# Kernel optimization log

Hardware: AMD Instinct MI355X
Metric: run time of the kernel (lower is better)

## Reference

```python
import jax, jax.numpy as jnp
import numpy as np

N, L, C, K = 8, 16384, 256, 64  # batch, points, d_color, anchor_num; d_struct = 4*K = 256


def setup_inputs() -> dict:
    key = jax.random.key(0)
    ks = jax.random.split(key, 12)
    d_in = C + 4 * K  # 512
    s1, s2, s3 = 1.0 / np.sqrt(d_in), 1.0 / np.sqrt(128), 1.0 / np.sqrt(256)
    return {
        'feat0': jax.random.normal(ks[0], (N, L, C), jnp.float32),
        'feat1': jax.random.normal(ks[1], (N, L, C), jnp.float32),
        'pts_3d0': jax.random.normal(ks[2], (N, L, 3), jnp.float32),
        'pts_3d1': jax.random.normal(ks[3], (N, L, 3), jnp.float32),
        'anchor_i': jax.random.randint(ks[4], (N, K), 0, L, jnp.int32),
        'anchor_j': jax.random.randint(ks[5], (N, K), 0, L, jnp.int32),
        'W1': jax.random.uniform(ks[6], (d_in, 128), jnp.float32, -s1, s1),
        'b1': jax.random.uniform(ks[7], (128,), jnp.float32, -s1, s1),
        'W2': jax.random.uniform(ks[8], (128, 256), jnp.float32, -s2, s2),
        'b2': jax.random.uniform(ks[9], (256,), jnp.float32, -s2, s2),
        'W3': jax.random.uniform(ks[10], (256, C), jnp.float32, -s3, s3),
        'b3': jax.random.uniform(ks[11], (C,), jnp.float32, -s3, s3),
    }


def _structured(pts, anchor_idx):
    # pts: [N,L,3], anchor_idx: [N,K] -> [N,L,4K]
    anchors = jnp.take_along_axis(pts, anchor_idx[:, :, None], axis=1)  # [N,K,3]
    diff = pts[:, :, None, :] - anchors[:, None, :, :]                  # [N,L,K,3]
    dist = jnp.sum(diff * diff, axis=-1, keepdims=True)                 # [N,L,K,1]
    f = jnp.concatenate([diff, dist], axis=-1)                          # [N,L,K,4]
    f = f / jnp.sum(jnp.abs(f), axis=-2, keepdims=True)                 # L1 norm over K
    f = jnp.swapaxes(f, -1, -2).reshape(pts.shape[0], pts.shape[1], -1)  # [N,L,4K]
    # original l1_norm is @torch.no_grad -> structured feature is detached
    return jax.lax.stop_gradient(f)


def _mlp(x, W1, b1, W2, b2, W3, b3):
    h = jax.nn.relu(x @ W1 + b1)
    h = jax.nn.relu(h @ W2 + b2)  # dropout is identity in eval
    return h @ W3 + b3


def reference(feat0, feat1, pts_3d0, pts_3d1, anchor_i, anchor_j,
              W1, b1, W2, b2, W3, b3):
    s0 = _structured(pts_3d0, anchor_i)
    s1 = _structured(pts_3d1, anchor_j)
    aug0 = _mlp(jnp.concatenate([feat0, s0], axis=-1), W1, b1, W2, b2, W3, b3)
    aug1 = _mlp(jnp.concatenate([feat1, s1], axis=-1), W1, b1, W2, b2, W3, b3)
    return aug0, aug1
```

## Files before the change

kernel.cpp:

```cpp
#include <hip/hip_runtime.h>

typedef __bf16 bf16x8 __attribute__((ext_vector_type(8)));
typedef float f32x4 __attribute__((ext_vector_type(4)));
typedef unsigned short u16x4 __attribute__((ext_vector_type(4)));

#define NBATCH 8
#define LPTS   16384
#define CDIM   256
#define KANC   64
#define DIN    512
#define H1DIM  128
#define H2DIM  256
#define TM     64
#define XSTR   320

__device__ __forceinline__ unsigned short f2b(float f){
  __bf16 h = (__bf16)f;
  return __builtin_bit_cast(unsigned short, h);
}

#define LBAR() do{ \
  asm volatile("s_waitcnt lgkmcnt(0)" ::: "memory"); \
  __builtin_amdgcn_s_barrier(); \
  asm volatile("" ::: "memory"); \
} while(0)

__global__ __launch_bounds__(256) void prep_weights(
    const float* __restrict__ W1, const float* __restrict__ W2,
    const float* __restrict__ W3, unsigned short* __restrict__ wt){
  int id = blockIdx.x * 256 + threadIdx.x;
  if (id < 65536){
    int r = id >> 9, c = id & 511;
    wt[id] = f2b(W1[c * 128 + r]);
  } else if (id < 98304){
    int t = id - 65536; int r = t >> 7, c = t & 127;
    wt[id] = f2b(W2[c * 256 + r]);
  } else if (id < 163840){
    int t = id - 98304; int r = t >> 8, c = t & 255;
    wt[id] = f2b(W3[c * 256 + r]);
  }
}

__global__ __launch_bounds__(128) void prep_coef(
    const float* __restrict__ pts0, const float* __restrict__ pts1,
    const int* __restrict__ anc_i, const int* __restrict__ anc_j,
    const float* __restrict__ W1, float* __restrict__ coef,
    unsigned short* __restrict__ cbf){
  const int comb = blockIdx.x;
  const int strm = comb >> 3, n = comb & 7;
  const int col  = threadIdx.x;
  __shared__ float4 anc[64];
  const float* pts  = strm ? pts1 : pts0;
  const int*   anci = strm ? anc_j : anc_i;
  if (col < 64){
    int ai = anci[n * KANC + col];
    const float* ap = pts + ((size_t)n * LPTS + ai) * 3;
    anc[col] = make_float4(ap[0], ap[1], ap[2], 0.f);
  }
  __syncthreads();
  float SX=0,CX=0,SY=0,CY=0,SZ=0,CZ=0,SD=0,ADx=0,ADy=0,ADz=0,CD2=0;
  float SAx=0,SAy=0,SAz=0,SA2=0;
  for (int k = 0; k < KANC; ++k){
    float4 a = anc[k];
    float ak2 = a.x*a.x + a.y*a.y + a.z*a.z;
    float wx = W1[(256 + k) * 128 + col];
    float wy = W1[(320 + k) * 128 + col];
    float wz = W1[(384 + k) * 128 + col];
    float wd = W1[(448 + k) * 128 + col];
    SX += wx; CX += a.x * wx;
    SY += wy; CY += a.y * wy;
    SZ += wz; CZ += a.z * wz;
    SD += wd; ADx += a.x * wd; ADy += a.y * wd; ADz += a.z * wd;
    CD2 += ak2 * wd;
    SAx += a.x; SAy += a.y; SAz += a.z; SA2 += ak2;
  }
  float* cf = coef + (size_t)comb * 12 * 128;
  cf[ 0*128+col]=SX;  cf[ 1*128+col]=CX;  cf[ 2*128+col]=SY;  cf[ 3*128+col]=CY;
  cf[ 4*128+col]=SZ;  cf[ 5*128+col]=CZ;  cf[ 6*128+col]=SD;  cf[ 7*128+col]=ADx;
  cf[ 8*128+col]=ADy; cf[ 9*128+col]=ADz; cf[10*128+col]=CD2;
  if (col == 0) cf[11*128+0] = SAx;
  if (col == 1) cf[11*128+1] = SAy;
  if (col == 2) cf[11*128+2] = SAz;
  if (col == 3) cf[11*128+3] = SA2;
  unsigned short* cb = cbf + ((size_t)comb * 128 + col) * 32;
  cb[0]=f2b(SX);  cb[1]=f2b(CX);  cb[2]=f2b(SY);  cb[3]=f2b(CY);
  cb[4]=f2b(SZ);  cb[5]=f2b(CZ);  cb[6]=f2b(SD);  cb[7]=f2b(ADx);
  cb[8]=f2b(ADy); cb[9]=f2b(ADz); cb[10]=f2b(CD2);
  #pragma unroll
  for (int j = 11; j < 32; ++j) cb[j] = 0;
}

__global__ __launch_bounds__(512, 4) void fused(
    const float* __restrict__ feat0, const float* __restrict__ feat1,
    const float* __restrict__ pts0, const float* __restrict__ pts1,
    const int* __restrict__ anc_i, const int* __restrict__ anc_j,
    const float* __restrict__ b1, const float* __restrict__ b2,
    const float* __restrict__ b3, const unsigned short* __restrict__ wt,
    const float* __restrict__ coef, const unsigned short* __restrict__ cbf,
    float* __restrict__ out)
{
  __shared__ unsigned short xs[TM * XSTR];
  __shared__ unsigned short h1s[TM * H1DIM];
  unsigned short* h2s = xs;

  const int tid  = threadIdx.x;
  const int wg   = blockIdx.x;
  const int strm = wg >> 11;
  const int n    = (wg >> 8) & 7;
  const int l0   = (wg & 255) * TM;
  const int comb = (strm << 3) | n;

  const float* feat = strm ? feat1 : feat0;
  const float* pts  = strm ? pts1 : pts0;
  const int*   anci = strm ? anc_j : anc_i;
  const float* cf   = coef + (size_t)comb * 12 * 128;

  const int lane = tid & 63;
  const int w    = tid >> 6;
  const int lr   = lane & 15;
  const int lg   = lane >> 4;
  const int col1 = w * 16 + lr;
  const int col0 = w * 32;
  const unsigned short* wrow1 = wt + col1 * DIN;
  const unsigned short* cbrow = cbf + ((size_t)comb * 128 + col1) * 32;
  const unsigned short* w2t = wt + 65536;
  const unsigned short* w3t = wt + 98304;

  float ax, ay, az;
  {
    int ai = anci[n * KANC + lane];
    const float* ap = pts + ((size_t)n * LPTS + ai) * 3;
    ax = ap[0]; ay = ap[1]; az = ap[2];
  }
  const float* pp = pts + ((size_t)n * LPTS + l0 + (tid >> 3)) * 3;
  float px = pp[0], py = pp[1], pz = pp[2];
  float SAx = cf[11*128+0], SAy = cf[11*128+1], SAz = cf[11*128+2], SA2 = cf[11*128+3];
  float bias1 = b1[col1];

  {
    const float4* fb = (const float4*)(feat + ((size_t)n * LPTS + l0) * CDIM);
    #pragma unroll
    for (int it = 0; it < 8; ++it){
      int flat = it * 512 + tid;
      int r = flat >> 6, c4 = flat & 63;
      float4 v = fb[flat];
      int e = (r * XSTR + c4 * 4) ^ ((r & 7) << 3);
      u16x4 pk = { f2b(v.x), f2b(v.y), f2b(v.z), f2b(v.w) };
      *(u16x4*)&xs[e] = pk;
    }
  }

  {
    const int l   = tid >> 3;
    const int sub = tid & 7;
    float s0 = 0.f, s1 = 0.f, s2 = 0.f;
    #pragma unroll
    for (int i = 0; i < 8; ++i){
      int src = sub * 8 + i;
      float akx = __shfl(ax, src, 64);
      float aky = __shfl(ay, src, 64);
      float akz = __shfl(az, src, 64);
      s0 += fabsf(px - akx); s1 += fabsf(py - aky); s2 += fabsf(pz - akz);
    }
    #pragma unroll
    for (int m = 1; m <= 4; m <<= 1){
      s0 += __shfl_xor(s0, m, 64);
      s1 += __shfl_xor(s1, m, 64);
      s2 += __shfl_xor(s2, m, 64);
    }
    float pp2 = px*px + py*py + pz*pz;
    float s3 = 64.f * pp2 - 2.f * (px*SAx + py*SAy + pz*SAz) + SA2;
    float i0 = 1.f/s0, i1 = 1.f/s1, i2 = 1.f/s2, i3 = 1.f/s3;
    float a0, a1, a2, a3;
    if (sub == 0){ a0 = i0*px;      a1 = -i0;       a2 = i1*py; a3 = -i1; }
    else if (sub == 1){ a0 = i2*pz; a1 = -i2;       a2 = i3*pp2; a3 = -2.f*i3*px; }
    else if (sub == 2){ a0 = -2.f*i3*py; a1 = -2.f*i3*pz; a2 = i3; a3 = 0.f; }
    else { a0 = a1 = a2 = a3 = 0.f; }
    int widx = (l * XSTR + 256 + sub * 4) ^ ((l & 7) << 3);
    u16x4 pk = { f2b(a0), f2b(a1), f2b(a2), f2b(a3) };
    *(u16x4*)&xs[widx] = pk;
  }
  LBAR();

  {
    f32x4 acc[4] = {};
    #pragma unroll
    for (int kk = 0; kk < 9; ++kk){
      int kb = kk * 32 + lg * 8;
      bf16x8 b = (kk < 8) ? *(const bf16x8*)&wrow1[kb]
                          : *(const bf16x8*)&cbrow[lg * 8];
      #pragma unroll
      for (int m = 0; m < 4; ++m){
        int row = m * 16 + lr;
        bf16x8 a = *(const bf16x8*)&xs[(row * XSTR + kb) ^ ((row & 7) << 3)];
        acc[m] = __builtin_amdgcn_mfma_f32_16x16x32_bf16(a, b, acc[m], 0, 0, 0);
      }
    }
    #pragma unroll
    for (int m = 0; m < 4; ++m){
      #pragma unroll
      for (int r = 0; r < 4; ++r){
        int row = m * 16 + lg * 4 + r;
        float v = fmaxf(acc[m][r] + bias1, 0.f);
        h1s[(row * H1DIM + col1) ^ ((row & 7) << 3)] = f2b(v);
      }
    }
  }
  LBAR();

  {
    f32x4 acc[4][2] = {};
    #pragma unroll
    for (int kk = 0; kk < 4; ++kk){
      int kb = kk * 32 + lg * 8;
      bf16x8 bf0 = *(const bf16x8*)&w2t[(col0 + lr) * H1DIM + kb];
      bf16x8 bf1 = *(const bf16x8*)&w2t[(col0 + 16 + lr) * H1DIM + kb];
      #pragma unroll
      for (int m = 0; m < 4; ++m){
        int row = m * 16 + lr;
        bf16x8 a = *(const bf16x8*)&h1s[(row * H1DIM + kb) ^ ((row & 7) << 3)];
        acc[m][0] = __builtin_amdgcn_mfma_f32_16x16x32_bf16(a, bf0, acc[m][0], 0, 0, 0);
        acc[m][1] = __builtin_amdgcn_mfma_f32_16x16x32_bf16(a, bf1, acc[m][1], 0, 0, 0);
      }
    }
    #pragma unroll
    for (int nt = 0; nt < 2; ++nt){
      int col = col0 + nt * 16 + lr;
      float bias = b2[col];
      #pragma unroll
      for (int m = 0; m < 4; ++m){
        #pragma unroll
        for (int r = 0; r < 4; ++r){
          int row = m * 16 + lg * 4 + r;
          float v = fmaxf(acc[m][nt][r] + bias, 0.f);
          h2s[(row * H2DIM + col) ^ ((row & 7) << 3)] = f2b(v);
        }
      }
    }
  }
  LBAR();

  {
    f32x4 acc[4][2] = {};
    #pragma unroll 4
    for (int kk = 0; kk < 8; ++kk){
      int kb = kk * 32 + lg * 8;
      bf16x8 bf0 = *(const bf16x8*)&w3t[(col0 + lr) * H2DIM + kb];
      bf16x8 bf1 = *(const bf16x8*)&w3t[(col0 + 16 + lr) * H2DIM + kb];
      #pragma unroll
      for (int m = 0; m < 4; ++m){
        int row = m * 16 + lr;
        bf16x8 a = *(const bf16x8*)&h2s[(row * H2DIM + kb) ^ ((row & 7) << 3)];
        acc[m][0] = __builtin_amdgcn_mfma_f32_16x16x32_bf16(a, bf0, acc[m][0], 0, 0, 0);
        acc[m][1] = __builtin_amdgcn_mfma_f32_16x16x32_bf16(a, bf1, acc[m][1], 0, 0, 0);
      }
    }
    float* ob = out + (((size_t)strm * NBATCH + n) * LPTS + l0) * CDIM;
    #pragma unroll
    for (int nt = 0; nt < 2; ++nt){
      int col = col0 + nt * 16 + lr;
      float bias = b3[col];
      #pragma unroll
      for (int m = 0; m < 4; ++m){
        #pragma unroll
        for (int r = 0; r < 4; ++r){
          int row = m * 16 + lg * 4 + r;
          ob[(size_t)row * CDIM + col] = acc[m][nt][r] + bias;
        }
      }
    }
  }
}

extern "C" void kernel_launch(void* const* d_in, const int* in_sizes, int n_in,
                              void* d_out, int out_size, void* d_ws, size_t ws_size,
                              hipStream_t stream){
  const float* feat0 = (const float*)d_in[0];
  const float* feat1 = (const float*)d_in[1];
  const float* pts0  = (const float*)d_in[2];
  const float* pts1  = (const float*)d_in[3];
  const int*   anci  = (const int*)d_in[4];
  const int*   ancj  = (const int*)d_in[5];
  const float* W1    = (const float*)d_in[6];
  const float* b1    = (const float*)d_in[7];
  const float* W2    = (const float*)d_in[8];
  const float* b2    = (const float*)d_in[9];
  const float* W3    = (const float*)d_in[10];
  const float* b3    = (const float*)d_in[11];
  unsigned short* wt = (unsigned short*)d_ws;
  float* coef = (float*)((char*)d_ws + 163840 * sizeof(unsigned short));
  unsigned short* cbf = (unsigned short*)((char*)d_ws + 163840 * 2 + 98304);
  float* out = (float*)d_out;

  prep_weights<<<640, 256, 0, stream>>>(W1, W2, W3, wt);
  prep_coef<<<16, 128, 0, stream>>>(pts0, pts1, anci, ancj, W1, coef, cbf);
  fused<<<4096, 512, 0, stream>>>(feat0, feat1, pts0, pts1, anci, ancj,
                                  b1, b2, b3, wt, coef, cbf, out);
}
```

Measured before the change: 217.0 us.

## Make fused MLP kernel persistent with producer/consumer warp specialization and double buffering

Converts the fused kernel into a persistent kernel of 1024 blocks that each process 8 tiles of 32 rows. Half the waves prefetch the next tile's features and compute its structured coefficients into a double-buffered LDS tile, while the other half run the three MFMA layers on the current tile. The aim is to overlap global loads with matrix compute and to keep weight fragments in registers. In exchange, fewer waves issue MFMAs, tiles are smaller, and more barriers are needed per tile.

Measured after the change: 752.4 us. 3.47x slower.

```diff
diff --git a/kernel.cpp b/kernel.cpp
--- a/kernel.cpp
+++ b/kernel.cpp
@@ -11,8 +11,10 @@
 #define DIN    512
 #define H1DIM  128
 #define H2DIM  256
-#define TM     64
-#define XSTR   320
+#define TM     32
+#define XSTR   288
+#define NBLK   1024
+#define ITERS  8
 
 __device__ __forceinline__ unsigned short f2b(float f){
   __bf16 h = (__bf16)f;
@@ -99,64 +101,50 @@
     const float* __restrict__ coef, const unsigned short* __restrict__ cbf,
     float* __restrict__ out)
 {
-  __shared__ unsigned short xs[TM * XSTR];
+  __shared__ unsigned short xs[2][TM * XSTR];
   __shared__ unsigned short h1s[TM * H1DIM];
-  unsigned short* h2s = xs;
+  __shared__ unsigned short h2s[TM * H2DIM];
 
   const int tid  = threadIdx.x;
   const int wg   = blockIdx.x;
-  const int strm = wg >> 11;
-  const int n    = (wg >> 8) & 7;
-  const int l0   = (wg & 255) * TM;
-  const int comb = (strm << 3) | n;
-
-  const float* feat = strm ? feat1 : feat0;
-  const float* pts  = strm ? pts1 : pts0;
-  const int*   anci = strm ? anc_j : anc_i;
-  const float* cf   = coef + (size_t)comb * 12 * 128;
+  const bool prod = (tid < 256);
 
   const int lane = tid & 63;
-  const int w    = tid >> 6;
   const int lr   = lane & 15;
   const int lg   = lane >> 4;
-  const int col1 = w * 16 + lr;
-  const int col0 = w * 32;
-  const unsigned short* wrow1 = wt + col1 * DIN;
-  const unsigned short* cbrow = cbf + ((size_t)comb * 128 + col1) * 32;
+  const int wq   = (tid & 255) >> 6;
   const unsigned short* w2t = wt + 65536;
   const unsigned short* w3t = wt + 98304;
 
-  float ax, ay, az;
-  {
+  const int pl   = (tid >> 3) & 31;
+  const int psub = tid & 7;
+
+  float4 fv[8];
+  float ua0 = 0.f, ua1 = 0.f, ua2 = 0.f, ua3 = 0.f;
+
+  if (prod){
+    int gt = wg;
+    int strm = gt >> 12, n = (gt >> 9) & 7, l0 = (gt & 511) * TM;
+    const float* feat = strm ? feat1 : feat0;
+    const float* pts  = strm ? pts1 : pts0;
+    const int*   anci = strm ? anc_j : anc_i;
+    const float* cf   = coef + (size_t)((strm << 3) | n) * 12 * 128;
+
+    const float4* fb = (const float4*)(feat + ((size_t)n * LPTS + l0) * CDIM);
+    #pragma unroll
+    for (int k = 0; k < 8; ++k) fv[k] = fb[k * 256 + tid];
+
     int ai = anci[n * KANC + lane];
     const float* ap = pts + ((size_t)n * LPTS + ai) * 3;
-    ax = ap[0]; ay = ap[1]; az = ap[2];
-  }
-  const float* pp = pts + ((size_t)n * LPTS + l0 + (tid >> 3)) * 3;
-  float px = pp[0], py = pp[1], pz = pp[2];
-  float SAx = cf[11*128+0], SAy = cf[11*128+1], SAz = cf[11*128+2], SA2 = cf[11*128+3];
-  float bias1 = b1[col1];
-
-  {
-    const float4* fb = (const float4*)(feat + ((size_t)n * LPTS + l0) * CDIM);
-    #pragma unroll
-    for (int it = 0; it < 8; ++it){
-      int flat = it * 512 + tid;
-      int r = flat >> 6, c4 = flat & 63;
-      float4 v = fb[flat];
-      int e = (r * XSTR + c4 * 4) ^ ((r & 7) << 3);
-      u16x4 pk = { f2b(v.x), f2b(v.y), f2b(v.z), f2b(v.w) };
-      *(u16x4*)&xs[e] = pk;
-    }
-  }
-
-  {
-    const int l   = tid >> 3;
-    const int sub = tid & 7;
+    float ax = ap[0], ay = ap[1], az = ap[2];
+    const float* pp = pts + ((size_t)n * LPTS + l0 + pl) * 3;
+    float px = pp[0], py = pp[1], pz = pp[2];
+    float SAx = cf[11*128+0], SAy = cf[11*128+1], SAz = cf[11*128+2], SA2 = cf[11*128+3];
+
     float s0 = 0.f, s1 = 0.f, s2 = 0.f;
     #pragma unroll
     for (int i = 0; i < 8; ++i){
-      int src = sub * 8 + i;
+      int src = psub * 8 + i;
       float akx = __shfl(ax, src, 64);
       float aky = __shfl(ay, src, 64);
       float akz = __shfl(az, src, 64);
@@ -172,102 +160,239 @@
     float s3 = 64.f * pp2 - 2.f * (px*SAx + py*SAy + pz*SAz) + SA2;
     float i0 = 1.f/s0, i1 = 1.f/s1, i2 = 1.f/s2, i3 = 1.f/s3;
     float a0, a1, a2, a3;
-    if (sub == 0){ a0 = i0*px;      a1 = -i0;       a2 = i1*py; a3 = -i1; }
-    else if (sub == 1){ a0 = i2*pz; a1 = -i2;       a2 = i3*pp2; a3 = -2.f*i3*px; }
-    else if (sub == 2){ a0 = -2.f*i3*py; a1 = -2.f*i3*pz; a2 = i3; a3 = 0.f; }
+    if (psub == 0){ a0 = i0*px; a1 = -i0; a2 = i1*py; a3 = -i1; }
+    else if (psub == 1){ a0 = i2*pz; a1 = -i2; a2 = i3*pp2; a3 = -2.f*i3*px; }
+    else if (psub == 2){ a0 = -2.f*i3*py; a1 = -2.f*i3*pz; a2 = i3; a3 = 0.f; }
     else { a0 = a1 = a2 = a3 = 0.f; }
-    int widx = (l * XSTR + 256 + sub * 4) ^ ((l & 7) << 3);
-    u16x4 pk = { f2b(a0), f2b(a1), f2b(a2), f2b(a3) };
-    *(u16x4*)&xs[widx] = pk;
-  }
-  LBAR();
-
-  {
-    f32x4 acc[4] = {};
+
     #pragma unroll
-    for (int kk = 0; kk < 9; ++kk){
-      int kb = kk * 32 + lg * 8;
-      bf16x8 b = (kk < 8) ? *(const bf16x8*)&wrow1[kb]
-                          : *(const bf16x8*)&cbrow[lg * 8];
-      #pragma unroll
-      for (int m = 0; m < 4; ++m){
-        int row = m * 16 + lr;
-        bf16x8 a = *(const bf16x8*)&xs[(row * XSTR + kb) ^ ((row & 7) << 3)];
-        acc[m] = __builtin_amdgcn_mfma_f32_16x16x32_bf16(a, b, acc[m], 0, 0, 0);
-      }
+    for (int k = 0; k < 8; ++k){
+      int flat = k * 256 + tid;
+      int r = flat >> 6, c4 = flat & 63;
+      float4 v = fv[k];
+      int e = (r * XSTR + c4 * 4) ^ ((r & 7) << 3);
+      u16x4 pk = { f2b(v.x), f2b(v.y), f2b(v.z), f2b(v.w) };
+      *(u16x4*)&xs[0][e] = pk;
     }
-    #pragma unroll
-    for (int m = 0; m < 4; ++m){
-      #pragma unroll
-      for (int r = 0; r < 4; ++r){
-        int row = m * 16 + lg * 4 + r;
-        float v = fmaxf(acc[m][r] + bias1, 0.f);
-        h1s[(row * H1DIM + col1) ^ ((row & 7) << 3)] = f2b(v);
-      }
+    {
+      int e = (pl * XSTR + 256 + psub * 4) ^ ((pl & 7) << 3);
+      u16x4 pk = { f2b(a0), f2b(a1), f2b(a2), f2b(a3) };
+      *(u16x4*)&xs[0][e] = pk;
     }
   }
   LBAR();
 
-  {
-    f32x4 acc[4][2] = {};
-    #pragma unroll
-    for (int kk = 0; kk < 4; ++kk){
-      int kb = kk * 32 + lg * 8;
-      bf16x8 bf0 = *(const bf16x8*)&w2t[(col0 + lr) * H1DIM + kb];
-      bf16x8 bf1 = *(const bf16x8*)&w2t[(col0 + 16 + lr) * H1DIM + kb];
-      #pragma unroll
-      for (int m = 0; m < 4; ++m){
-        int row = m * 16 + lr;
-        bf16x8 a = *(const bf16x8*)&h1s[(row * H1DIM + kb) ^ ((row & 7) << 3)];
-        acc[m][0] = __builtin_amdgcn_mfma_f32_16x16x32_bf16(a, bf0, acc[m][0], 0, 0, 0);
-        acc[m][1] = __builtin_amdgcn_mfma_f32_16x16x32_bf16(a, bf1, acc[m][1], 0, 0, 0);
+  #pragma unroll 1
+  for (int it = 0; it < ITERS; ++it){
+    const int cur = it & 1;
+    const int gt = it * NBLK + wg;
+    const int strm = gt >> 12, n = (gt >> 9) & 7, l0 = (gt & 511) * TM;
+    const int comb = (strm << 3) | n;
+
+    if (prod){
+      if (it < ITERS - 1){
+        int gtn = gt + NBLK;
+        int strmN = gtn >> 12, nN = (gtn >> 9) & 7, l0N = (gtn & 511) * TM;
+        const float* featN = strmN ? feat1 : feat0;
+        const float* ptsN  = strmN ? pts1 : pts0;
+        const int*   anciN = strmN ? anc_j : anc_i;
+        const float* cfN   = coef + (size_t)((strmN << 3) | nN) * 12 * 128;
+
+        const float4* fb = (const float4*)(featN + ((size_t)nN * LPTS + l0N) * CDIM);
+        #pragma unroll
+        for (int k = 0; k < 8; ++k) fv[k] = fb[k * 256 + tid];
+
+        int ai = anciN[nN * KANC + lane];
+        const float* ap = ptsN + ((size_t)nN * LPTS + ai) * 3;
+        float ax = ap[0], ay = ap[1], az = ap[2];
+        const float* pp = ptsN + ((size_t)nN * LPTS + l0N + pl) * 3;
+        float px = pp[0], py = pp[1], pz = pp[2];
+        float SAx = cfN[11*128+0], SAy = cfN[11*128+1], SAz = cfN[11*128+2], SA2 = cfN[11*128+3];
+
+        float s0 = 0.f, s1 = 0.f, s2 = 0.f;
+        #pragma unroll
+        for (int i = 0; i < 8; ++i){
+          int src = psub * 8 + i;
+          float akx = __shfl(ax, src, 64);
+          float aky = __shfl(ay, src, 64);
+          float akz = __shfl(az, src, 64);
+          s0 += fabsf(px - akx); s1 += fabsf(py - aky); s2 += fabsf(pz - akz);
+        }
+        #pragma unroll
+        for (int m = 1; m <= 4; m <<= 1){
+          s0 += __shfl_xor(s0, m, 64);
+          s1 += __shfl_xor(s1, m, 64);
+          s2 += __shfl_xor(s2, m, 64);
+        }
+        float pp2 = px*px + py*py + pz*pz;
+        float s3 = 64.f * pp2 - 2.f * (px*SAx + py*SAy + pz*SAz) + SA2;
+        float i0 = 1.f/s0, i1 = 1.f/s1, i2 = 1.f/s2, i3 = 1.f/s3;
+        if (psub == 0){ ua0 = i0*px; ua1 = -i0; ua2 = i1*py; ua3 = -i1; }
+        else if (psub == 1){ ua0 = i2*pz; ua1 = -i2; ua2 = i3*pp2; ua3 = -2.f*i3*px; }
+        else if (psub == 2){ ua0 = -2.f*i3*py; ua1 = -2.f*i3*pz; ua2 = i3; ua3 = 0.f; }
+        else { ua0 = ua1 = ua2 = ua3 = 0.f; }
       }
-    }
-    #pragma unroll
-    for (int nt = 0; nt < 2; ++nt){
-      int col = col0 + nt * 16 + lr;
-      float bias = b2[col];
-      #pragma unroll
-      for (int m = 0; m < 4; ++m){
-        #pragma unroll
-        for (int r = 0; r < 4; ++r){
-          int row = m * 16 + lg * 4 + r;
-          float v = fmaxf(acc[m][nt][r] + bias, 0.f);
-          h2s[(row * H2DIM + col) ^ ((row & 7) << 3)] = f2b(v);
-        }
+      LBAR();
+      if (it < ITERS - 1){
+        unsigned short* xw = xs[cur ^ 1];
+        #pragma unroll
+        for (int k = 0; k < 8; ++k){
+          int flat = k * 256 + tid;
+          int r = flat >> 6, c4 = flat & 63;
+          float4 v = fv[k];
+          int e = (r * XSTR + c4 * 4) ^ ((r & 7) << 3);
+          u16x4 pk = { f2b(v.x), f2b(v.y), f2b(v.z), f2b(v.w) };
+          *(u16x4*)&xw[e] = pk;
+        }
+        int e = (pl * XSTR + 256 + psub * 4) ^ ((pl & 7) << 3);
+        u16x4 pk = { f2b(ua0), f2b(ua1), f2b(ua2), f2b(ua3) };
+        *(u16x4*)&xw[e] = pk;
       }
-    }
-  }
-  LBAR();
-
-  {
-    f32x4 acc[4][2] = {};
-    #pragma unroll 4
-    for (int kk = 0; kk < 8; ++kk){
-      int kb = kk * 32 + lg * 8;
-      bf16x8 bf0 = *(const bf16x8*)&w3t[(col0 + lr) * H2DIM + kb];
-      bf16x8 bf1 = *(const bf16x8*)&w3t[(col0 + 16 + lr) * H2DIM + kb];
-      #pragma unroll
-      for (int m = 0; m < 4; ++m){
-        int row = m * 16 + lr;
-        bf16x8 a = *(const bf16x8*)&h2s[(row * H2DIM + kb) ^ ((row & 7) << 3)];
-        acc[m][0] = __builtin_amdgcn_mfma_f32_16x16x32_bf16(a, bf0, acc[m][0], 0, 0, 0);
-        acc[m][1] = __builtin_amdgcn_mfma_f32_16x16x32_bf16(a, bf1, acc[m][1], 0, 0, 0);
+      LBAR();
+      LBAR();
+    } else {
+      const unsigned short* xr = xs[cur];
+      {
+        const int colA = wq * 32 + lr, colB = colA + 16;
+        const unsigned short* wrA = wt + colA * DIN;
+        const unsigned short* wrB = wt + colB * DIN;
+        const unsigned short* cbA = cbf + ((size_t)comb * 128 + colA) * 32;
+        const unsigned short* cbB = cbf + ((size_t)comb * 128 + colB) * 32;
+        float biasA = b1[colA], biasB = b1[colB];
+        bf16x8 bb[18];
+        #pragma unroll
+        for (int kk = 0; kk < 8; ++kk){
+          int kb = kk * 32 + lg * 8;
+          bb[kk * 2    ] = *(const bf16x8*)&wrA[kb];
+          bb[kk * 2 + 1] = *(const bf16x8*)&wrB[kb];
+        }
+        bb[16] = *(const bf16x8*)&cbA[lg * 8];
+        bb[17] = *(const bf16x8*)&cbB[lg * 8];
+        f32x4 acc[2][2] = {};
+        #pragma unroll
+        for (int kk = 0; kk < 9; ++kk){
+          int kb = kk * 32 + lg * 8;
+          #pragma unroll
+          for (int m = 0; m < 2; ++m){
+            int row = m * 16 + lr;
+            bf16x8 a = *(const bf16x8*)&xr[(row * XSTR + kb) ^ ((row & 7) << 3)];
+            acc[m][0] = __builtin_amdgcn_mfma_f32_16x16x32_bf16(a, bb[kk*2  ], acc[m][0], 0, 0, 0);
+            acc[m][1] = __builtin_amdgcn_mfma_f32_16x16x32_bf16(a, bb[kk*2+1], acc[m][1], 0, 0, 0);
+          }
+        }
+        #pragma unroll
+        for (int nt = 0; nt < 2; ++nt){
+          int col = nt ? colB : colA;
+          float bias = nt ? biasB : biasA;
+          #pragma unroll
+          for (int m = 0; m < 2; ++m){
+            #pragma unroll
+            for (int r = 0; r < 4; ++r){
+              int row = m * 16 + lg * 4 + r;
+              float v = fmaxf(acc[m][nt][r] + bias, 0.f);
+              h1s[(row * H1DIM + col) ^ ((row & 7) << 3)] = f2b(v);
+            }
+          }
+        }
       }
-    }
-    float* ob = out + (((size_t)strm * NBATCH + n) * LPTS + l0) * CDIM;
-    #pragma unroll
-    for (int nt = 0; nt < 2; ++nt){
-      int col = col0 + nt * 16 + lr;
-      float bias = b3[col];
-      #pragma unroll
-      for (int m = 0; m < 4; ++m){
-        #pragma unroll
-        for (int r = 0; r < 4; ++r){
-          int row = m * 16 + lg * 4 + r;
-          ob[(size_t)row * CDIM + col] = acc[m][nt][r] + bias;
+      LBAR();
+      {
+        const int colG = wq * 64;
+        bf16x8 bb[16];
+        #pragma unroll
+        for (int kk = 0; kk < 4; ++kk){
+          int kb = kk * 32 + lg * 8;
+          #pragma unroll
+          for (int nt = 0; nt < 4; ++nt)
+            bb[kk * 4 + nt] = *(const bf16x8*)&w2t[(colG + nt * 16 + lr) * H1DIM + kb];
+        }
+        f32x4 acc[2][4] = {};
+        #pragma unroll
+        for (int kk = 0; kk < 4; ++kk){
+          int kb = kk * 32 + lg * 8;
+          #pragma unroll
+          for (int m = 0; m < 2; ++m){
+            int row = m * 16 + lr;
+            bf16x8 a = *(const bf16x8*)&h1s[(row * H1DIM + kb) ^ ((row & 7) << 3)];
+            #pragma unroll
+            for (int nt = 0; nt < 4; ++nt)
+              acc[m][nt] = __builtin_amdgcn_mfma_f32_16x16x32_bf16(a, bb[kk*4+nt], acc[m][nt], 0, 0, 0);
+          }
+        }
+        #pragma unroll
+        for (int nt = 0; nt < 4; ++nt){
+          int col = colG + nt * 16 + lr;
+          float bias = b2[col];
+          #pragma unroll
+          for (int m = 0; m < 2; ++m){
+            #pragma unroll
+            for (int r = 0; r < 4; ++r){
+              int row = m * 16 + lg * 4 + r;
+              float v = fmaxf(acc[m][nt][r] + bias, 0.f);
+              h2s[(row * H2DIM + col) ^ ((row & 7) << 3)] = f2b(v);
+            }
+          }
         }
       }
+      LBAR();
+      {
+        const int colG = wq * 64;
+        f32x4 acc[2][4] = {};
+        bf16x8 bb[16];
+        #pragma unroll
+        for (int kk = 0; kk < 4; ++kk){
+          int kb = kk * 32 + lg * 8;
+          #pragma unroll
+          for (int nt = 0; nt < 4; ++nt)
+            bb[kk * 4 + nt] = *(const bf16x8*)&w3t[(colG + nt * 16 + lr) * H2DIM + kb];
+        }
+        #pragma unroll
+        for (int kk = 0; kk < 4; ++kk){
+          int kb = kk * 32 + lg * 8;
+          #pragma unroll
+          for (int m = 0; m < 2; ++m){
+            int row = m * 16 + lr;
+            bf16x8 a = *(const bf16x8*)&h2s[(row * H2DIM + kb) ^ ((row & 7) << 3)];
+            #pragma unroll
+            for (int nt = 0; nt < 4; ++nt)
+              acc[m][nt] = __builtin_amdgcn_mfma_f32_16x16x32_bf16(a, bb[kk*4+nt], acc[m][nt], 0, 0, 0);
+          }
+        }
+        #pragma unroll
+        for (int kk = 0; kk < 4; ++kk){
+          int kb = (kk + 4) * 32 + lg * 8;
+          #pragma unroll
+          for (int nt = 0; nt < 4; ++nt)
+            bb[kk * 4 + nt] = *(const bf16x8*)&w3t[(colG + nt * 16 + lr) * H2DIM + kb];
+        }
+        #pragma unroll
+        for (int kk = 0; kk < 4; ++kk){
+          int kb = (kk + 4) * 32 + lg * 8;
+          #pragma unroll
+          for (int m = 0; m < 2; ++m){
+            int row = m * 16 + lr;
+            bf16x8 a = *(const bf16x8*)&h2s[(row * H2DIM + kb) ^ ((row & 7) << 3)];
+            #pragma unroll
+            for (int nt = 0; nt < 4; ++nt)
+              acc[m][nt] = __builtin_amdgcn_mfma_f32_16x16x32_bf16(a, bb[kk*4+nt], acc[m][nt], 0, 0, 0);
+          }
+        }
+        float* ob = out + (((size_t)strm * NBATCH + n) * LPTS + l0) * CDIM;
+        #pragma unroll
+        for (int nt = 0; nt < 4; ++nt){
+          int col = colG + nt * 16 + lr;
+          float bias = b3[col];
+          #pragma unroll
+          for (int m = 0; m < 2; ++m){
+            #pragma unroll
+            for (int r = 0; r < 4; ++r){
+              int row = m * 16 + lg * 4 + r;
+              ob[(size_t)row * CDIM + col] = acc[m][nt][r] + bias;
+            }
+          }
+        }
+      }
+      LBAR();
     }
   }
 }
@@ -294,6 +419,6 @@
 
   prep_weights<<<640, 256, 0, stream>>>(W1, W2, W3, wt);
   prep_coef<<<16, 128, 0, stream>>>(pts0, pts1, anci, ancj, W1, coef, cbf);
-  fused<<<4096, 512, 0, stream>>>(feat0, feat1, pts0, pts1, anci, ancj,
+  fused<<<NBLK, 512, 0, stream>>>(feat0, feat1, pts0, pts1, anci, ancj,
                                   b1, b2, b3, wt, coef, cbf, out);
 }
```
